# Kernel tuning notes

Measured on AMD Instinct MI355X. Metric: run time of the kernel, lower is better.

Reference implementation:

```python
import jax, jax.numpy as jnp
import numpy as np

B, NS, NT, E, K, D = 4, 10000, 10000, 160000, 16, 128


def _layer_norm(x, g, b, eps=1e-5):
    m = jnp.mean(x, axis=-1, keepdims=True)
    v = jnp.mean(jnp.square(x - m), axis=-1, keepdims=True)
    return (x - m) * jax.lax.rsqrt(v + eps) * g + b


def setup_inputs() -> dict:
    key = jax.random.key(0)
    ks = jax.random.split(key, 12)
    return {
        "bond_embedding": jax.random.normal(ks[0], (B, E, D), jnp.float32),
        "src_embedding": jax.random.normal(ks[1], (B, NS, D), jnp.float32),
        "tgt_embedding": jax.random.normal(ks[2], (B, NT, D), jnp.float32),
        "W_s2e": jax.random.normal(ks[3], (D, D), jnp.float32) * (1.0 / np.sqrt(D)),
        "W_t2e": jax.random.normal(ks[4], (D, D), jnp.float32) * (1.0 / np.sqrt(D)),
        "W_e2e": jax.random.normal(ks[5], (D, D), jnp.float32) * (1.0 / np.sqrt(D)),
        "ln1_g": jnp.ones((D,), jnp.float32),
        "ln1_b": jnp.zeros((D,), jnp.float32),
        "W_e2t": jax.random.normal(ks[6], (D, D), jnp.float32) * (1.0 / np.sqrt(D)),
        "W_t2t": jax.random.normal(ks[7], (D, D), jnp.float32) * (1.0 / np.sqrt(D)),
        "ln2_g": jnp.ones((D,), jnp.float32),
        "ln2_b": jnp.zeros((D,), jnp.float32),
        "bond_coef": jax.random.uniform(ks[8], (NT, K), jnp.float32),
        "src_order": jax.random.randint(ks[9], (E,), 0, NS, jnp.int32),
        "tgt_order": jax.random.randint(ks[10], (E,), 0, NT, jnp.int32),
        "edge_order": jax.random.randint(ks[11], (NT, K), 0, E, jnp.int32),
    }


def reference(bond_embedding, src_embedding, tgt_embedding,
              W_s2e, W_t2e, W_e2e, ln1_g, ln1_b,
              W_e2t, W_t2t, ln2_g, ln2_b,
              bond_coef, src_order, tgt_order, edge_order):
    # node2bond: project nodes then gather onto edges, sum with bond projection
    d_bond = (src_embedding @ W_s2e)[:, src_order]            # [B,E,D]
    d_bond = d_bond + (tgt_embedding @ W_t2e)[:, tgt_order]   # [B,E,D]
    d_bond = d_bond + bond_embedding @ W_e2e
    d_bond = _layer_norm(jax.nn.silu(d_bond), ln1_g, ln1_b)
    # bond2node: gather edges per target node, weighted mean over K
    gathered = d_bond[:, edge_order] * bond_coef[None, :, :, None]  # [B,NT,K,D]
    bond_reduce = gathered.mean(axis=-2)                            # [B,NT,D]
    d_tgt = bond_reduce @ W_e2t + tgt_embedding @ W_t2t
    d_tgt = _layer_norm(jax.nn.silu(d_tgt), ln2_g, ln2_b)
    return (bond_embedding + d_bond, src_embedding, tgt_embedding + d_tgt)
```

## Files before the change

### kernel.cpp

```cpp
#include <hip/hip_runtime.h>
#include <hip/hip_bf16.h>
#include <stdint.h>

#define BB   4
#define NS   10000
#define NT   10000
#define EE   160000
#define KK   16
#define DD   128

typedef short s8v  __attribute__((ext_vector_type(8)));
typedef float f4v  __attribute__((ext_vector_type(4)));

static __device__ __forceinline__ float bf2f(unsigned short u) {
    union { unsigned int i; float f; } v; v.i = ((unsigned int)u) << 16; return v.f;
}
static __device__ __forceinline__ unsigned short f2bf(float f) {
    union { float f; unsigned int i; } v; v.f = f;
    unsigned int x = v.i;
    unsigned int r = x + 0x7fffu + ((x >> 16) & 1u);
    return (unsigned short)(r >> 16);
}

static __device__ __forceinline__ s8v load_bfrag_f32(const float* __restrict__ W,
                                                     int c, int t, int q, int np) {
    s8v r;
    const float* p = W + (32 * c + 8 * q) * DD + 16 * t + np;
#pragma unroll
    for (int j = 0; j < 8; ++j) r[j] = (short)f2bf(p[j * DD]);
    return r;
}

static __device__ __forceinline__ s8v load_afrag_f32(const float* __restrict__ p) {
    s8v r;
#pragma unroll
    for (int j = 0; j < 8; ++j) r[j] = (short)f2bf(p[j]);
    return r;
}

__global__ __launch_bounds__(256, 2)
void proj_kernel(const float* __restrict__ src,
                 const float* __restrict__ tgt,
                 const float* __restrict__ Ws,
                 const float* __restrict__ Wt,
                 unsigned short* __restrict__ out_s,
                 unsigned short* __restrict__ out_t)
{
    const int lane = threadIdx.x & 63;
    const int wave = threadIdx.x >> 6;
    const int np = lane & 15, q = lane >> 4;

    const float* X; const float* W; unsigned short* O;
    if (blockIdx.y == 0) { X = src; W = Ws; O = out_s; }
    else                 { X = tgt; W = Wt; O = out_t; }

    s8v bw[4][8];
#pragma unroll
    for (int c = 0; c < 4; ++c)
#pragma unroll
        for (int t = 0; t < 8; ++t) bw[c][t] = load_bfrag_f32(W, c, t, q, np);

    const int NTILES = (BB * NS) / 16;
    const int nw = gridDim.x * 4;
    for (int tile = blockIdx.x * 4 + wave; tile < NTILES; tile += nw) {
        const float* abase = X + (size_t)(tile * 16 + np) * DD + 8 * q;
        s8v a[4];
#pragma unroll
        for (int c = 0; c < 4; ++c) a[c] = load_afrag_f32(abase + 32 * c);
        f4v acc[8];
        const f4v zero = {0.f, 0.f, 0.f, 0.f};
#pragma unroll
        for (int t = 0; t < 8; ++t) acc[t] = zero;
#pragma unroll
        for (int c = 0; c < 4; ++c)
#pragma unroll
            for (int t = 0; t < 8; ++t)
                acc[t] = __builtin_amdgcn_mfma_f32_16x16x32_bf16(a[c], bw[c][t], acc[t], 0, 0, 0);
        const size_t orow = (size_t)(tile * 16 + 4 * q) * DD;
#pragma unroll
        for (int r = 0; r < 4; ++r)
#pragma unroll
            for (int t = 0; t < 8; ++t)
                O[orow + (size_t)r * DD + 16 * t + np] = f2bf(acc[t][r]);
    }
}

__global__ __launch_bounds__(256, 2)
void bond_kernel(const float* __restrict__ bond,
                 const float* __restrict__ We,
                 const unsigned short* __restrict__ sproj,
                 const unsigned short* __restrict__ tproj,
                 const int* __restrict__ src_order,
                 const int* __restrict__ tgt_order,
                 const float* __restrict__ g1,
                 const float* __restrict__ b1,
                 float* __restrict__ out0,
                 unsigned short* __restrict__ dbond)
{
    const int lane = threadIdx.x & 63;
    const int wave = threadIdx.x >> 6;
    const int np = lane & 15, q = lane >> 4;
    const int b = blockIdx.y;

    s8v bw[4][8];
#pragma unroll
    for (int c = 0; c < 4; ++c)
#pragma unroll
        for (int t = 0; t < 8; ++t) bw[c][t] = load_bfrag_f32(We, c, t, q, np);

    float gv[8], bv[8];
#pragma unroll
    for (int t = 0; t < 8; ++t) { gv[t] = g1[16 * t + np]; bv[t] = b1[16 * t + np]; }

    const int TPB = EE / 16;
    const int nw = gridDim.x * 4;
    for (int tile = blockIdx.x * 4 + wave; tile < TPB; tile += nw) {
        const int e0 = tile * 16;
        const size_t rowbase = ((size_t)b * EE + e0) * DD;

        const float* abase = bond + rowbase + (size_t)np * DD + 8 * q;
        s8v a[4];
#pragma unroll
        for (int c = 0; c < 4; ++c) a[c] = load_afrag_f32(abase + 32 * c);

        f4v acc[8];
        const f4v zero = {0.f, 0.f, 0.f, 0.f};
#pragma unroll
        for (int t = 0; t < 8; ++t) acc[t] = zero;
#pragma unroll
        for (int c = 0; c < 4; ++c)
#pragma unroll
            for (int t = 0; t < 8; ++t)
                acc[t] = __builtin_amdgcn_mfma_f32_16x16x32_bf16(a[c], bw[c][t], acc[t], 0, 0, 0);

        float s1[4] = {0.f, 0.f, 0.f, 0.f};
        float s2[4] = {0.f, 0.f, 0.f, 0.f};
#pragma unroll
        for (int r = 0; r < 4; ++r) {
            const int e = e0 + 4 * q + r;
            const int se = src_order[e];
            const int te = tgt_order[e];
            const unsigned short* sp = sproj + ((size_t)b * NS + se) * DD + np;
            const unsigned short* tp = tproj + ((size_t)b * NT + te) * DD + np;
#pragma unroll
            for (int t = 0; t < 8; ++t) {
                float d = acc[t][r] + bf2f(sp[16 * t]) + bf2f(tp[16 * t]);
                float s = 1.0f / (1.0f + __expf(-d));
                float xv = d * s;
                acc[t][r] = xv;
                s1[r] += xv;
                s2[r] += xv * xv;
            }
        }
#pragma unroll
        for (int off = 1; off < 16; off <<= 1) {
#pragma unroll
            for (int r = 0; r < 4; ++r) {
                s1[r] += __shfl_xor(s1[r], off, 16);
                s2[r] += __shfl_xor(s2[r], off, 16);
            }
        }
        float mean[4], rstd[4];
#pragma unroll
        for (int r = 0; r < 4; ++r) {
            mean[r] = s1[r] * (1.0f / 128.0f);
            float var = s2[r] * (1.0f / 128.0f) - mean[r] * mean[r];
            rstd[r] = rsqrtf(var + 1e-5f);
        }
        const size_t crow = rowbase + (size_t)(4 * q) * DD;
#pragma unroll
        for (int r = 0; r < 4; ++r) {
            const size_t ro = crow + (size_t)r * DD;
#pragma unroll
            for (int t = 0; t < 8; ++t) {
                float y = (acc[t][r] - mean[r]) * rstd[r] * gv[t] + bv[t];
                const int col = 16 * t + np;
                out0[ro + col] = bond[ro + col] + y;
                if (dbond) dbond[ro + col] = f2bf(y);
            }
        }
    }
}

__global__ __launch_bounds__(256, 2)
void tgt_kernel(const unsigned short* __restrict__ dbond,
                const float* __restrict__ out0,
                const float* __restrict__ bond,
                const float* __restrict__ tgt,
                const float* __restrict__ We2t,
                const float* __restrict__ Wt2t,
                const float* __restrict__ coef,
                const int* __restrict__ edge_order,
                const float* __restrict__ g2,
                const float* __restrict__ b2,
                float* __restrict__ out2)
{
    const int lane = threadIdx.x & 63;
    const int wave = threadIdx.x >> 6;
    const int np = lane & 15, q = lane >> 4;
    const int b = blockIdx.y;

    const int tile = blockIdx.x * 4 + wave;
    if (tile >= NT / 16) return;
    const int t0 = tile * 16;
    const int myrow = t0 + np;

    float ad[4][8];
#pragma unroll
    for (int c = 0; c < 4; ++c)
#pragma unroll
        for (int j = 0; j < 8; ++j) ad[c][j] = 0.f;

    for (int k = 0; k < KK; ++k) {
        const int eo = edge_order[myrow * KK + k];
        const float cf = coef[myrow * KK + k];
        if (dbond) {
            const unsigned short* p = dbond + ((size_t)b * EE + eo) * DD + 8 * q;
#pragma unroll
            for (int c = 0; c < 4; ++c)
#pragma unroll
                for (int j = 0; j < 8; ++j)
                    ad[c][j] += cf * bf2f(p[32 * c + j]);
        } else {
            const float* p0 = out0 + ((size_t)b * EE + eo) * DD + 8 * q;
            const float* p1 = bond + ((size_t)b * EE + eo) * DD + 8 * q;
#pragma unroll
            for (int c = 0; c < 4; ++c)
#pragma unroll
                for (int j = 0; j < 8; ++j)
                    ad[c][j] += cf * (p0[32 * c + j] - p1[32 * c + j]);
        }
    }
    s8v adf[4];
#pragma unroll
    for (int c = 0; c < 4; ++c)
#pragma unroll
        for (int j = 0; j < 8; ++j) adf[c][j] = (short)f2bf(ad[c][j] * (1.0f / 16.0f));

    const float* tb = tgt + ((size_t)b * NT + myrow) * DD + 8 * q;
    s8v at[4];
#pragma unroll
    for (int c = 0; c < 4; ++c) at[c] = load_afrag_f32(tb + 32 * c);

    f4v acc[8];
    const f4v zero = {0.f, 0.f, 0.f, 0.f};
#pragma unroll
    for (int t = 0; t < 8; ++t) acc[t] = zero;
#pragma unroll
    for (int c = 0; c < 4; ++c) {
#pragma unroll
        for (int t = 0; t < 8; ++t) {
            acc[t] = __builtin_amdgcn_mfma_f32_16x16x32_bf16(adf[c], load_bfrag_f32(We2t, c, t, q, np), acc[t], 0, 0, 0);
            acc[t] = __builtin_amdgcn_mfma_f32_16x16x32_bf16(at[c],  load_bfrag_f32(Wt2t, c, t, q, np), acc[t], 0, 0, 0);
        }
    }

    float gv[8], bv[8];
#pragma unroll
    for (int t = 0; t < 8; ++t) { gv[t] = g2[16 * t + np]; bv[t] = b2[16 * t + np]; }

    float s1[4] = {0.f, 0.f, 0.f, 0.f};
    float s2[4] = {0.f, 0.f, 0.f, 0.f};
#pragma unroll
    for (int r = 0; r < 4; ++r)
#pragma unroll
        for (int t = 0; t < 8; ++t) {
            float d = acc[t][r];
            float s = 1.0f / (1.0f + __expf(-d));
            float xv = d * s;
            acc[t][r] = xv;
            s1[r] += xv;
            s2[r] += xv * xv;
        }
#pragma unroll
    for (int off = 1; off < 16; off <<= 1) {
#pragma unroll
        for (int r = 0; r < 4; ++r) {
            s1[r] += __shfl_xor(s1[r], off, 16);
            s2[r] += __shfl_xor(s2[r], off, 16);
        }
    }
    float mean[4], rstd[4];
#pragma unroll
    for (int r = 0; r < 4; ++r) {
        mean[r] = s1[r] * (1.0f / 128.0f);
        float var = s2[r] * (1.0f / 128.0f) - mean[r] * mean[r];
        rstd[r] = rsqrtf(var + 1e-5f);
    }
    const size_t crow = ((size_t)b * NT + t0 + 4 * q) * DD;
#pragma unroll
    for (int r = 0; r < 4; ++r) {
        const size_t ro = crow + (size_t)r * DD;
#pragma unroll
        for (int t = 0; t < 8; ++t) {
            float y = (acc[t][r] - mean[r]) * rstd[r] * gv[t] + bv[t];
            const int col = 16 * t + np;
            out2[ro + col] = tgt[ro + col] + y;
        }
    }
}

__global__ void copy_kernel(const uint4* __restrict__ s, uint4* __restrict__ d, int n) {
    int i = blockIdx.x * blockDim.x + threadIdx.x;
    const int st = gridDim.x * blockDim.x;
    for (; i < n; i += st) d[i] = s[i];
}

extern "C" void kernel_launch(void* const* d_in, const int* in_sizes, int n_in,
                              void* d_out, int out_size, void* d_ws, size_t ws_size,
                              hipStream_t stream)
{
    const float* bond = (const float*)d_in[0];
    const float* src  = (const float*)d_in[1];
    const float* tgt  = (const float*)d_in[2];
    const float* Ws2e = (const float*)d_in[3];
    const float* Wt2e = (const float*)d_in[4];
    const float* We2e = (const float*)d_in[5];
    const float* g1   = (const float*)d_in[6];
    const float* b1   = (const float*)d_in[7];
    const float* We2t = (const float*)d_in[8];
    const float* Wt2t = (const float*)d_in[9];
    const float* g2   = (const float*)d_in[10];
    const float* b2   = (const float*)d_in[11];
    const float* coef = (const float*)d_in[12];
    const int* src_order  = (const int*)d_in[13];
    const int* tgt_order  = (const int*)d_in[14];
    const int* edge_order = (const int*)d_in[15];

    float* out0 = (float*)d_out;
    float* out1 = out0 + (size_t)BB * EE * DD;
    float* out2 = out1 + (size_t)BB * NS * DD;

    unsigned short* sproj = (unsigned short*)out1;
    unsigned short* tproj = (unsigned short*)out2;

    const size_t dbond_bytes = (size_t)BB * EE * DD * 2;
    unsigned short* dbond = (ws_size >= dbond_bytes) ? (unsigned short*)d_ws : nullptr;

    proj_kernel<<<dim3(128, 2), 256, 0, stream>>>(src, tgt, Ws2e, Wt2e, sproj, tproj);

    bond_kernel<<<dim3(128, BB), 256, 0, stream>>>(bond, We2e, sproj, tproj,
                                                   src_order, tgt_order, g1, b1,
                                                   out0, dbond);

    tgt_kernel<<<dim3(157, BB), 256, 0, stream>>>(dbond, out0, bond, tgt, We2t, Wt2t,
                                                  coef, edge_order, g2, b2, out2);

    copy_kernel<<<dim3(1024), 256, 0, stream>>>((const uint4*)src, (uint4*)out1,
                                                (int)((size_t)BB * NS * DD / 4));
}
```

Baseline: 1.047 ms.

## Prepack weight fragments, vectorize gathers, permute projection layout, use nontemporal stores

Adds a small prep kernel that converts the five weight matrices to bf16 MFMA B-fragments once. Kernels then read each fragment with one 16-byte load instead of doing per-wave strided fp32 loads and conversions. The source/target projection outputs are stored in a permuted column order, so the bond kernel can gather each row with one s8v load per lane; the edge and order indices are also read as int4 and the dbond gather uses 16-byte vectors. Output stores and the copy become nontemporal, launch bounds rise to 4 blocks per CU, and the proj and bond grids grow. The cost is an extra launch, fragment loads from global memory inside the MFMA loop, and scratch space in the unused half of the src output buffer.

```diff
diff --git a/kernel.cpp b/kernel.cpp
--- a/kernel.cpp
+++ b/kernel.cpp
@@ -1,5 +1,4 @@
 #include <hip/hip_runtime.h>
-#include <hip/hip_bf16.h>
 #include <stdint.h>
 
 #define BB   4
@@ -11,6 +10,7 @@
 
 typedef short s8v  __attribute__((ext_vector_type(8)));
 typedef float f4v  __attribute__((ext_vector_type(4)));
+typedef unsigned int u4v __attribute__((ext_vector_type(4)));
 
 static __device__ __forceinline__ float bf2f(unsigned short u) {
     union { unsigned int i; float f; } v; v.i = ((unsigned int)u) << 16; return v.f;
@@ -22,43 +22,60 @@
     return (unsigned short)(r >> 16);
 }
 
-static __device__ __forceinline__ s8v load_bfrag_f32(const float* __restrict__ W,
-                                                     int c, int t, int q, int np) {
+static __device__ __forceinline__ s8v load_afrag_f32(const float* __restrict__ p) {
+    const float4 v0 = *(const float4*)(p);
+    const float4 v1 = *(const float4*)(p + 4);
     s8v r;
-    const float* p = W + (32 * c + 8 * q) * DD + 16 * t + np;
-#pragma unroll
-    for (int j = 0; j < 8; ++j) r[j] = (short)f2bf(p[j * DD]);
+    r[0] = (short)f2bf(v0.x); r[1] = (short)f2bf(v0.y);
+    r[2] = (short)f2bf(v0.z); r[3] = (short)f2bf(v0.w);
+    r[4] = (short)f2bf(v1.x); r[5] = (short)f2bf(v1.y);
+    r[6] = (short)f2bf(v1.z); r[7] = (short)f2bf(v1.w);
     return r;
 }
 
-static __device__ __forceinline__ s8v load_afrag_f32(const float* __restrict__ p) {
-    s8v r;
-#pragma unroll
-    for (int j = 0; j < 8; ++j) r[j] = (short)f2bf(p[j]);
-    return r;
-}
-
-__global__ __launch_bounds__(256, 2)
-void proj_kernel(const float* __restrict__ src,
-                 const float* __restrict__ tgt,
-                 const float* __restrict__ Ws,
-                 const float* __restrict__ Wt,
-                 unsigned short* __restrict__ out_s,
-                 unsigned short* __restrict__ out_t)
-{
+#define WFRAG_U16 (32 * 64 * 8)
+
+__global__ void wprep_kernel(const float* __restrict__ W0, const float* __restrict__ W1,
+                             const float* __restrict__ W2, const float* __restrict__ W3,
+                             const float* __restrict__ W4, unsigned short* __restrict__ out)
+{
+    const float* W;
+    switch (blockIdx.x) {
+        case 0: W = W0; break;
+        case 1: W = W1; break;
+        case 2: W = W2; break;
+        case 3: W = W3; break;
+        default: W = W4; break;
+    }
+    unsigned short* O = out + (size_t)blockIdx.x * WFRAG_U16;
     const int lane = threadIdx.x & 63;
     const int wave = threadIdx.x >> 6;
     const int np = lane & 15, q = lane >> 4;
-
-    const float* X; const float* W; unsigned short* O;
-    if (blockIdx.y == 0) { X = src; W = Ws; O = out_s; }
-    else                 { X = tgt; W = Wt; O = out_t; }
-
-    s8v bw[4][8];
-#pragma unroll
-    for (int c = 0; c < 4; ++c)
-#pragma unroll
-        for (int t = 0; t < 8; ++t) bw[c][t] = load_bfrag_f32(W, c, t, q, np);
+    for (int ct = wave; ct < 32; ct += 4) {
+        const int c = ct >> 3, t = ct & 7;
+        const float* p = W + (32 * c + 8 * q) * DD + 16 * t + np;
+        s8v v;
+#pragma unroll
+        for (int j = 0; j < 8; ++j) v[j] = (short)f2bf(p[j * DD]);
+        *(s8v*)(O + ((size_t)ct * 64 + lane) * 8) = v;
+    }
+}
+
+__global__ __launch_bounds__(256, 4)
+void proj_kernel(const float* __restrict__ src,
+                 const float* __restrict__ tgt,
+                 const s8v* __restrict__ wfS,
+                 const s8v* __restrict__ wfT,
+                 unsigned short* __restrict__ out_s,
+                 unsigned short* __restrict__ out_t)
+{
+    const int lane = threadIdx.x & 63;
+    const int wave = threadIdx.x >> 6;
+    const int np = lane & 15, q = lane >> 4;
+
+    const float* X; const s8v* wf; unsigned short* O;
+    if (blockIdx.y == 0) { X = src; wf = wfS; O = out_s; }
+    else                 { X = tgt; wf = wfT; O = out_t; }
 
     const int NTILES = (BB * NS) / 16;
     const int nw = gridDim.x * 4;
@@ -75,19 +92,20 @@
         for (int c = 0; c < 4; ++c)
 #pragma unroll
             for (int t = 0; t < 8; ++t)
-                acc[t] = __builtin_amdgcn_mfma_f32_16x16x32_bf16(a[c], bw[c][t], acc[t], 0, 0, 0);
-        const size_t orow = (size_t)(tile * 16 + 4 * q) * DD;
-#pragma unroll
-        for (int r = 0; r < 4; ++r)
-#pragma unroll
-            for (int t = 0; t < 8; ++t)
-                O[orow + (size_t)r * DD + 16 * t + np] = f2bf(acc[t][r]);
-    }
-}
-
-__global__ __launch_bounds__(256, 2)
+                acc[t] = __builtin_amdgcn_mfma_f32_16x16x32_bf16(a[c], wf[(c * 8 + t) * 64 + lane], acc[t], 0, 0, 0);
+#pragma unroll
+        for (int r = 0; r < 4; ++r) {
+            s8v v;
+#pragma unroll
+            for (int t = 0; t < 8; ++t) v[t] = (short)f2bf(acc[t][r]);
+            *(s8v*)(O + (size_t)(tile * 16 + 4 * q + r) * DD + np * 8) = v;
+        }
+    }
+}
+
+__global__ __launch_bounds__(256, 4)
 void bond_kernel(const float* __restrict__ bond,
-                 const float* __restrict__ We,
+                 const s8v* __restrict__ wfE,
                  const unsigned short* __restrict__ sproj,
                  const unsigned short* __restrict__ tproj,
                  const int* __restrict__ src_order,
@@ -102,12 +120,6 @@
     const int np = lane & 15, q = lane >> 4;
     const int b = blockIdx.y;
 
-    s8v bw[4][8];
-#pragma unroll
-    for (int c = 0; c < 4; ++c)
-#pragma unroll
-        for (int t = 0; t < 8; ++t) bw[c][t] = load_bfrag_f32(We, c, t, q, np);
-
     float gv[8], bv[8];
 #pragma unroll
     for (int t = 0; t < 8; ++t) { gv[t] = g1[16 * t + np]; bv[t] = b1[16 * t + np]; }
@@ -123,6 +135,17 @@
 #pragma unroll
         for (int c = 0; c < 4; ++c) a[c] = load_afrag_f32(abase + 32 * c);
 
+        const int4 se4 = *(const int4*)(src_order + e0 + 4 * q);
+        const int4 te4 = *(const int4*)(tgt_order + e0 + 4 * q);
+        const int se[4] = {se4.x, se4.y, se4.z, se4.w};
+        const int te[4] = {te4.x, te4.y, te4.z, te4.w};
+        s8v gs[4], gt[4];
+#pragma unroll
+        for (int r = 0; r < 4; ++r) {
+            gs[r] = *(const s8v*)(sproj + ((size_t)b * NS + se[r]) * DD + np * 8);
+            gt[r] = *(const s8v*)(tproj + ((size_t)b * NT + te[r]) * DD + np * 8);
+        }
+
         f4v acc[8];
         const f4v zero = {0.f, 0.f, 0.f, 0.f};
 #pragma unroll
@@ -131,20 +154,15 @@
         for (int c = 0; c < 4; ++c)
 #pragma unroll
             for (int t = 0; t < 8; ++t)
-                acc[t] = __builtin_amdgcn_mfma_f32_16x16x32_bf16(a[c], bw[c][t], acc[t], 0, 0, 0);
+                acc[t] = __builtin_amdgcn_mfma_f32_16x16x32_bf16(a[c], wfE[(c * 8 + t) * 64 + lane], acc[t], 0, 0, 0);
 
         float s1[4] = {0.f, 0.f, 0.f, 0.f};
         float s2[4] = {0.f, 0.f, 0.f, 0.f};
 #pragma unroll
         for (int r = 0; r < 4; ++r) {
-            const int e = e0 + 4 * q + r;
-            const int se = src_order[e];
-            const int te = tgt_order[e];
-            const unsigned short* sp = sproj + ((size_t)b * NS + se) * DD + np;
-            const unsigned short* tp = tproj + ((size_t)b * NT + te) * DD + np;
 #pragma unroll
             for (int t = 0; t < 8; ++t) {
-                float d = acc[t][r] + bf2f(sp[16 * t]) + bf2f(tp[16 * t]);
+                float d = acc[t][r] + bf2f((unsigned short)gs[r][t]) + bf2f((unsigned short)gt[r][t]);
                 float s = 1.0f / (1.0f + __expf(-d));
                 float xv = d * s;
                 acc[t][r] = xv;
@@ -175,20 +193,20 @@
             for (int t = 0; t < 8; ++t) {
                 float y = (acc[t][r] - mean[r]) * rstd[r] * gv[t] + bv[t];
                 const int col = 16 * t + np;
-                out0[ro + col] = bond[ro + col] + y;
-                if (dbond) dbond[ro + col] = f2bf(y);
-            }
-        }
-    }
-}
-
-__global__ __launch_bounds__(256, 2)
+                __builtin_nontemporal_store(bond[ro + col] + y, &out0[ro + col]);
+                if (dbond) __builtin_nontemporal_store(f2bf(y), &dbond[ro + col]);
+            }
+        }
+    }
+}
+
+__global__ __launch_bounds__(256, 4)
 void tgt_kernel(const unsigned short* __restrict__ dbond,
                 const float* __restrict__ out0,
                 const float* __restrict__ bond,
                 const float* __restrict__ tgt,
-                const float* __restrict__ We2t,
-                const float* __restrict__ Wt2t,
+                const s8v* __restrict__ wfE2T,
+                const s8v* __restrict__ wfT2T,
                 const float* __restrict__ coef,
                 const int* __restrict__ edge_order,
                 const float* __restrict__ g2,
@@ -211,24 +229,36 @@
 #pragma unroll
         for (int j = 0; j < 8; ++j) ad[c][j] = 0.f;
 
-    for (int k = 0; k < KK; ++k) {
-        const int eo = edge_order[myrow * KK + k];
-        const float cf = coef[myrow * KK + k];
+    for (int kc = 0; kc < 4; ++kc) {
+        const int4   e4 = *(const int4*)(edge_order + myrow * KK + 4 * kc);
+        const float4 c4 = *(const float4*)(coef + myrow * KK + 4 * kc);
+        const int   eo[4] = {e4.x, e4.y, e4.z, e4.w};
+        const float cfv[4] = {c4.x, c4.y, c4.z, c4.w};
         if (dbond) {
-            const unsigned short* p = dbond + ((size_t)b * EE + eo) * DD + 8 * q;
-#pragma unroll
-            for (int c = 0; c < 4; ++c)
-#pragma unroll
-                for (int j = 0; j < 8; ++j)
-                    ad[c][j] += cf * bf2f(p[32 * c + j]);
+#pragma unroll
+            for (int k = 0; k < 4; ++k) {
+                const s8v* p = (const s8v*)(dbond + ((size_t)b * EE + eo[k]) * DD);
+                const float cf = cfv[k];
+#pragma unroll
+                for (int c = 0; c < 4; ++c) {
+                    const s8v v = p[4 * c + q];
+#pragma unroll
+                    for (int j = 0; j < 8; ++j)
+                        ad[c][j] += cf * bf2f((unsigned short)v[j]);
+                }
+            }
         } else {
-            const float* p0 = out0 + ((size_t)b * EE + eo) * DD + 8 * q;
-            const float* p1 = bond + ((size_t)b * EE + eo) * DD + 8 * q;
-#pragma unroll
-            for (int c = 0; c < 4; ++c)
-#pragma unroll
-                for (int j = 0; j < 8; ++j)
-                    ad[c][j] += cf * (p0[32 * c + j] - p1[32 * c + j]);
+#pragma unroll
+            for (int k = 0; k < 4; ++k) {
+                const float* p0 = out0 + ((size_t)b * EE + eo[k]) * DD + 8 * q;
+                const float* p1 = bond + ((size_t)b * EE + eo[k]) * DD + 8 * q;
+                const float cf = cfv[k];
+#pragma unroll
+                for (int c = 0; c < 4; ++c)
+#pragma unroll
+                    for (int j = 0; j < 8; ++j)
+                        ad[c][j] += cf * (p0[32 * c + j] - p1[32 * c + j]);
+            }
         }
     }
     s8v adf[4];
@@ -250,8 +280,8 @@
     for (int c = 0; c < 4; ++c) {
 #pragma unroll
         for (int t = 0; t < 8; ++t) {
-            acc[t] = __builtin_amdgcn_mfma_f32_16x16x32_bf16(adf[c], load_bfrag_f32(We2t, c, t, q, np), acc[t], 0, 0, 0);
-            acc[t] = __builtin_amdgcn_mfma_f32_16x16x32_bf16(at[c],  load_bfrag_f32(Wt2t, c, t, q, np), acc[t], 0, 0, 0);
+            acc[t] = __builtin_amdgcn_mfma_f32_16x16x32_bf16(adf[c], wfE2T[(c * 8 + t) * 64 + lane], acc[t], 0, 0, 0);
+            acc[t] = __builtin_amdgcn_mfma_f32_16x16x32_bf16(at[c],  wfT2T[(c * 8 + t) * 64 + lane], acc[t], 0, 0, 0);
         }
     }
 
@@ -295,15 +325,18 @@
         for (int t = 0; t < 8; ++t) {
             float y = (acc[t][r] - mean[r]) * rstd[r] * gv[t] + bv[t];
             const int col = 16 * t + np;
-            out2[ro + col] = tgt[ro + col] + y;
-        }
-    }
-}
-
-__global__ void copy_kernel(const uint4* __restrict__ s, uint4* __restrict__ d, int n) {
+            __builtin_nontemporal_store(tgt[ro + col] + y, &out2[ro + col]);
+        }
+    }
+}
+
+__global__ void copy_kernel(const u4v* __restrict__ s, u4v* __restrict__ d, int n) {
     int i = blockIdx.x * blockDim.x + threadIdx.x;
     const int st = gridDim.x * blockDim.x;
-    for (; i < n; i += st) d[i] = s[i];
+    for (; i < n; i += st) {
+        u4v v = __builtin_nontemporal_load(&s[i]);
+        __builtin_nontemporal_store(v, &d[i]);
+    }
 }
 
 extern "C" void kernel_launch(void* const* d_in, const int* in_sizes, int n_in,
@@ -334,18 +367,27 @@
     unsigned short* sproj = (unsigned short*)out1;
     unsigned short* tproj = (unsigned short*)out2;
 
+    unsigned short* wfrag = (unsigned short*)out1 + (size_t)BB * NS * DD;
+
     const size_t dbond_bytes = (size_t)BB * EE * DD * 2;
     unsigned short* dbond = (ws_size >= dbond_bytes) ? (unsigned short*)d_ws : nullptr;
 
-    proj_kernel<<<dim3(128, 2), 256, 0, stream>>>(src, tgt, Ws2e, Wt2e, sproj, tproj);
-
-    bond_kernel<<<dim3(128, BB), 256, 0, stream>>>(bond, We2e, sproj, tproj,
+    wprep_kernel<<<dim3(5), 256, 0, stream>>>(Ws2e, Wt2e, We2e, We2t, Wt2t, wfrag);
+    const s8v* wfS   = (const s8v*)(wfrag + 0 * (size_t)WFRAG_U16);
+    const s8v* wfT   = (const s8v*)(wfrag + 1 * (size_t)WFRAG_U16);
+    const s8v* wfE   = (const s8v*)(wfrag + 2 * (size_t)WFRAG_U16);
+    const s8v* wfE2T = (const s8v*)(wfrag + 3 * (size_t)WFRAG_U16);
+    const s8v* wfT2T = (const s8v*)(wfrag + 4 * (size_t)WFRAG_U16);
+
+    proj_kernel<<<dim3(157, 2), 256, 0, stream>>>(src, tgt, wfS, wfT, sproj, tproj);
+
+    bond_kernel<<<dim3(256, BB), 256, 0, stream>>>(bond, wfE, sproj, tproj,
                                                    src_order, tgt_order, g1, b1,
                                                    out0, dbond);
 
-    tgt_kernel<<<dim3(157, BB), 256, 0, stream>>>(dbond, out0, bond, tgt, We2t, Wt2t,
+    tgt_kernel<<<dim3(157, BB), 256, 0, stream>>>(dbond, out0, bond, tgt, wfE2T, wfT2T,
                                                   coef, edge_order, g2, b2, out2);
 
-    copy_kernel<<<dim3(1024), 256, 0, stream>>>((const uint4*)src, (uint4*)out1,
+    copy_kernel<<<dim3(1024), 256, 0, stream>>>((const u4v*)src, (u4v*)out1,
                                                 (int)((size_t)BB * NS * DD / 4));
 }
```

After: 1.221 ms. 1.17x slower.
